# Optimization experiments

Measured on AMD Instinct MI355X. Metric: run time of the kernel, lower is better.

Reference implementation:

```python
import jax, jax.numpy as jnp
import numpy as np

B, S, HID = 1, 2048, 2048
NH, NKV, HD = 16, 4, 128
G = NH // NKV  # queries per kv head (repeat_interleave factor)
QPA = 128      # query_pre_attn_scalar
EPS = 1e-6
SCALE = QPA ** -0.5
NEG = -1e9


def rms_norm(x, w, eps=EPS):
    return x * jax.lax.rsqrt(jnp.mean(x * x, axis=-1, keepdims=True) + eps) * w


def rope(x, cos, sin):
    # x: [B,S,H,D]; cos/sin: [S,D/2].
    # torch apply_rotary_emb: complex (x[:d/2] + i*x[d/2:]) * (cos + i*sin),
    # real parts -> first half, imag parts -> second half.
    d2 = x.shape[-1] // 2
    x1, x2 = x[..., :d2], x[..., d2:]
    c = cos[None, :, None, :]
    s = sin[None, :, None, :]
    return jnp.concatenate([x1 * c - x2 * s, x1 * s + x2 * c], axis=-1)


def setup_inputs() -> dict:
    key = jax.random.key(0)
    ks = jax.random.split(key, 4)
    hidden_states = jax.random.normal(ks[0], (B, S, HID), jnp.float32)
    inv_freq = 1.0 / (10000.0 ** (jnp.arange(0, HD, 2, dtype=jnp.float32) / HD))
    ang = jnp.arange(S, dtype=jnp.float32)[:, None] * inv_freq[None, :]  # [S, D/2]
    cos, sin = jnp.cos(ang), jnp.sin(ang)
    kv_write_indices = jnp.arange(S, dtype=jnp.int32)
    k_cache = jnp.zeros((B, S, NKV, HD), jnp.float32)
    v_cache = jnp.zeros((B, S, NKV, HD), jnp.float32)
    causal = jnp.tril(jnp.ones((S, S), dtype=bool))
    mask = jnp.where(causal, 0.0, NEG).astype(jnp.float32)[None, None]  # [1,1,S,S]
    qkv_out = (NH + 2 * NKV) * HD
    wqkv = jax.random.normal(ks[1], (qkv_out, HID), jnp.float32) * 0.02
    bqkv = jnp.zeros((qkv_out,), jnp.float32)
    wo = jax.random.normal(ks[2], (HID, NH * HD), jnp.float32) * 0.02
    bo = jnp.zeros((HID,), jnp.float32)
    q_norm_w = jnp.ones((HD,), jnp.float32)
    k_norm_w = jnp.ones((HD,), jnp.float32)
    return {"hidden_states": hidden_states, "cos": cos, "sin": sin,
            "k_cache": k_cache, "v_cache": v_cache, "mask": mask,
            "wqkv": wqkv, "bqkv": bqkv, "wo": wo, "bo": bo,
            "q_norm_w": q_norm_w, "k_norm_w": k_norm_w,
            "kv_write_indices": kv_write_indices}


def reference(hidden_states, cos, sin, k_cache, v_cache, mask,
              wqkv, bqkv, wo, bo, q_norm_w, k_norm_w, kv_write_indices):
    qkv = hidden_states @ wqkv.T + bqkv  # [B,S,(NH+2*NKV)*HD]
    q_sz, kv_sz = NH * HD, NKV * HD
    xq = qkv[..., :q_sz].reshape(B, S, NH, HD)
    xk = qkv[..., q_sz:q_sz + kv_sz].reshape(B, S, NKV, HD)
    xv = qkv[..., q_sz + kv_sz:].reshape(B, S, NKV, HD)
    xq = rope(rms_norm(xq, q_norm_w), cos, sin)
    xk = rope(rms_norm(xk, k_norm_w), cos, sin)
    k = k_cache.at[:, kv_write_indices].set(xk)  # index_copy_ on dim 1
    v = v_cache.at[:, kv_write_indices].set(xv)
    # GQA: head h attends with kv head h // G (repeat_interleave order)
    q = (xq * SCALE).reshape(B, S, NKV, G, HD)
    scores = jnp.einsum('bskgd,btkd->bkgst', q, k) + mask[:, :, None]  # [B,NKV,G,S,T]
    p = jax.nn.softmax(scores.astype(jnp.float32), axis=-1).astype(q.dtype)
    out = jnp.einsum('bkgst,btkd->bskgd', p, v).reshape(B, S, NH * HD)
    return out @ wo.T + bo
```

## Files before the change

kernel.cpp:

```cpp
#include <hip/hip_runtime.h>
#include <stdint.h>

#define S_LEN 2048
#define HIDN  2048
#define NH    16
#define NKV   4
#define HD    128
#define QKV_N 3072
#define Q_SZ  2048
#define SCALE_Q 0.088388347648318447f

typedef __attribute__((ext_vector_type(8))) short  short8;
typedef __attribute__((ext_vector_type(4))) float  f32x4;

__device__ __forceinline__ uint16_t f2bf(float f) {
  uint32_t u = __float_as_uint(f);
  u += 0x7fffu + ((u >> 16) & 1u);
  return (uint16_t)(u >> 16);
}

__device__ __forceinline__ void gload16(const void* g, void* lds_wave_base) {
  __builtin_amdgcn_global_load_lds(
      (const __attribute__((address_space(1))) uint32_t*)(uintptr_t)g,
      (__attribute__((address_space(3))) uint32_t*)(uint32_t)(uintptr_t)lds_wave_base,
      16, 0, 0);
}

__global__ __launch_bounds__(256) void cvt_kernel(const float* __restrict__ in,
                                                  uint16_t* __restrict__ out, int n) {
  int i = (blockIdx.x * 256 + threadIdx.x) * 4;
  if (i < n) {
    float4 v = *(const float4*)(in + i);
    ushort4 o;
    o.x = f2bf(v.x); o.y = f2bf(v.y); o.z = f2bf(v.z); o.w = f2bf(v.w);
    *(ushort4*)(out + i) = o;
  }
}

#define BM 128
#define BN 128
#define BK 64
__global__ __launch_bounds__(256) void gemm_nt(const uint16_t* __restrict__ A,
                                               const uint16_t* __restrict__ B,
                                               const float* __restrict__ bias,
                                               float* __restrict__ C,
                                               int M, int N, int K) {
  __shared__ uint16_t As[BM * BK];
  __shared__ uint16_t Bs[BN * BK];
  const int tid = threadIdx.x;
  const int m0 = blockIdx.y * BM;
  const int n0 = blockIdx.x * BN;
  const int lane = tid & 63;
  const int w = tid >> 6;
  const int wm = (w >> 1) * 64, wn = (w & 1) * 64;
  const int lr = lane & 15, lg = lane >> 4;
  const int wb = w << 10;
  const int lb = wb + lane * 16;

  f32x4 acc[4][4];
#pragma unroll
  for (int i = 0; i < 4; ++i)
#pragma unroll
    for (int j = 0; j < 4; ++j) acc[i][j] = (f32x4){0.f, 0.f, 0.f, 0.f};

  for (int k0 = 0; k0 < K; k0 += BK) {
#pragma unroll
    for (int i = 0; i < 4; ++i) {
      int b = i * 4096 + lb;
      int row = b >> 7;
      int colb = b & 127;
      gload16((const char*)A + ((size_t)(m0 + row) * K + k0) * 2 + colb,
              (char*)As + i * 4096 + wb);
      gload16((const char*)B + ((size_t)(n0 + row) * K + k0) * 2 + colb,
              (char*)Bs + i * 4096 + wb);
    }
    __syncthreads();
#pragma unroll
    for (int ks = 0; ks < 2; ++ks) {
      short8 av[4], bv[4];
#pragma unroll
      for (int i = 0; i < 4; ++i)
        av[i] = *(const short8*)(As + (wm + i * 16 + lr) * BK + ks * 32 + lg * 8);
#pragma unroll
      for (int j = 0; j < 4; ++j)
        bv[j] = *(const short8*)(Bs + (wn + j * 16 + lr) * BK + ks * 32 + lg * 8);
#pragma unroll
      for (int i = 0; i < 4; ++i)
#pragma unroll
        for (int j = 0; j < 4; ++j)
          acc[i][j] = __builtin_amdgcn_mfma_f32_16x16x32_bf16(av[i], bv[j], acc[i][j], 0, 0, 0);
    }
    __syncthreads();
  }
#pragma unroll
  for (int i = 0; i < 4; ++i) {
#pragma unroll
    for (int j = 0; j < 4; ++j) {
      int col = n0 + wn + j * 16 + lr;
      float bb = bias ? bias[col] : 0.f;
#pragma unroll
      for (int r = 0; r < 4; ++r) {
        int rowg = m0 + wm + i * 16 + lg * 4 + r;
        C[(size_t)rowg * N + col] = acc[i][j][r] + bb;
      }
    }
  }
}

__global__ __launch_bounds__(256) void qk_post(const float* __restrict__ qkv,
                                               const float* __restrict__ cosb,
                                               const float* __restrict__ sinb,
                                               const float* __restrict__ qw,
                                               const float* __restrict__ kw,
                                               const int* __restrict__ widx,
                                               uint16_t* __restrict__ Qo,
                                               uint16_t* __restrict__ Ko) {
  int row = blockIdx.x * 4 + (threadIdx.x >> 6);
  int lane = threadIdx.x & 63;
  int t = row / 20, head = row % 20;
  bool isq = head < NH;
  int off = isq ? head * HD : Q_SZ + (head - NH) * HD;
  const float* x = qkv + (size_t)t * QKV_N + off;
  float x1 = x[lane], x2 = x[lane + 64];
  float ss = x1 * x1 + x2 * x2;
#pragma unroll
  for (int m = 1; m < 64; m <<= 1) ss += __shfl_xor(ss, m, 64);
  float rs = rsqrtf(ss * (1.0f / 128.0f) + 1e-6f);
  const float* wn_ = isq ? qw : kw;
  float n1 = x1 * rs * wn_[lane], n2 = x2 * rs * wn_[lane + 64];
  float c = cosb[t * 64 + lane], s = sinb[t * 64 + lane];
  float o1 = n1 * c - n2 * s;
  float o2 = n1 * s + n2 * c;
  if (isq) {
    o1 *= SCALE_Q; o2 *= SCALE_Q;
    uint16_t* dst = Qo + ((size_t)t * NH + head) * HD;
    dst[lane] = f2bf(o1); dst[lane + 64] = f2bf(o2);
  } else {
    int td = widx[t];
    uint16_t* dst = Ko + ((size_t)td * NKV + (head - NH)) * HD;
    dst[lane] = f2bf(o1); dst[lane + 64] = f2bf(o2);
  }
}

__global__ __launch_bounds__(256) void vtrans(const float* __restrict__ qkv,
                                              const int* __restrict__ widx,
                                              uint16_t* __restrict__ Vt) {
  int b = blockIdx.x;
  int dt = b & 1;
  int tt = (b >> 1) & 31;
  int kh = b >> 6;
  __shared__ float tile[64][68];
  int tid = threadIdx.x;
  int r = tid >> 2, c0 = tid & 3;
  const float* src = qkv + (size_t)(tt * 64 + r) * QKV_N + Q_SZ + NKV * HD + kh * HD + dt * 64;
#pragma unroll
  for (int i = 0; i < 4; ++i) {
    float4 v = *(const float4*)(src + (c0 + i * 4) * 4);
    *(float4*)&tile[r][(c0 + i * 4) * 4] = v;
  }
  __syncthreads();
  int rd = tid >> 2;
#pragma unroll
  for (int j = 0; j < 16; ++j) {
    int tloc = c0 * 16 + j;
    int tg = widx[tt * 64 + tloc];
    Vt[(size_t)(kh * HD + dt * 64 + rd) * S_LEN + tg] = f2bf(tile[tloc][rd]);
  }
}

__global__ __launch_bounds__(256) void attn_kernel(const uint16_t* __restrict__ Q,
                                                   const uint16_t* __restrict__ Kc,
                                                   const uint16_t* __restrict__ Vt,
                                                   uint16_t* __restrict__ O) {
  __shared__ uint16_t Ks[64 * 128];
  __shared__ uint16_t Vs[128 * 64];
  __shared__ uint16_t Ps[4][16 * 136];
  __shared__ float Bc[4][16];

  const int h = blockIdx.y, kh = h >> 2;
  const int q0 = blockIdx.x * 64;
  const int tid = threadIdx.x, w = tid >> 6, lane = tid & 63;
  const int lr = lane & 15, lg = lane >> 4;
  const int qw0 = q0 + w * 16;
  const int wb = w << 10, lb = wb + lane * 16;

  short8 qf[4];
  const uint16_t* qb = Q + ((size_t)(qw0 + lr) * NH + h) * HD;
#pragma unroll
  for (int ks = 0; ks < 4; ++ks) qf[ks] = *(const short8*)(qb + ks * 32 + lg * 8);

  f32x4 o[8];
#pragma unroll
  for (int d = 0; d < 8; ++d) o[d] = (f32x4){0.f, 0.f, 0.f, 0.f};
  float mrun = -1e30f, lrun = 0.f;
  const int qg = qw0 + lr;

  const int ntiles = q0 / 64 + 1;
  for (int tt = 0; tt < ntiles; ++tt) {
    const int t0 = tt * 64;
#pragma unroll
    for (int i = 0; i < 4; ++i) {
      int b = i * 4096 + lb;
      int rowK = b >> 8, colK = b & 255;
      gload16((const char*)Kc + (((size_t)(t0 + rowK) * NKV + kh) * HD) * 2 + (colK ^ ((rowK & 7) << 4)),
              (char*)Ks + i * 4096 + wb);
      int rowV = b >> 7, colV = b & 127;
      gload16((const char*)Vt + ((size_t)(kh * HD + rowV) * S_LEN + t0) * 2 + (colV ^ ((rowV & 7) << 4)),
              (char*)Vs + i * 4096 + wb);
    }
    __syncthreads();

    f32x4 st[4];
#pragma unroll
    for (int ts = 0; ts < 4; ++ts) {
      st[ts] = (f32x4){0.f, 0.f, 0.f, 0.f};
#pragma unroll
      for (int ks = 0; ks < 4; ++ks) {
        int row = ts * 16 + lr;
        int cb = (ks * 64 + lg * 16) ^ ((row & 7) << 4);
        short8 kf = *(const short8*)((const char*)Ks + row * 256 + cb);
        st[ts] = __builtin_amdgcn_mfma_f32_16x16x32_bf16(kf, qf[ks], st[ts], 0, 0, 0);
      }
    }

    float pv[4][4];
    float pm = -1e30f;
#pragma unroll
    for (int ts = 0; ts < 4; ++ts)
#pragma unroll
      for (int r = 0; r < 4; ++r) {
        int tglob = t0 + ts * 16 + lg * 4 + r;
        float sv = (tglob > qg) ? -1e9f : st[ts][r];
        pv[ts][r] = sv;
        pm = fmaxf(pm, sv);
      }
    pm = fmaxf(pm, __shfl_xor(pm, 16, 64));
    pm = fmaxf(pm, __shfl_xor(pm, 32, 64));
    float mnew = fmaxf(mrun, pm);
    float scl = __expf(mrun - mnew);
    float psum = 0.f;
#pragma unroll
    for (int ts = 0; ts < 4; ++ts)
#pragma unroll
      for (int r = 0; r < 4; ++r) {
        pv[ts][r] = __expf(pv[ts][r] - mnew);
        psum += pv[ts][r];
      }
    psum += __shfl_xor(psum, 16, 64);
    psum += __shfl_xor(psum, 32, 64);
    lrun = lrun * scl + psum;
    mrun = mnew;
    if (lg == 0) Bc[w][lr] = scl;

    {
      uint32_t* pw = (uint32_t*)&Ps[w][0];
#pragma unroll
      for (int ts = 0; ts < 4; ++ts)
#pragma unroll
        for (int rr = 0; rr < 2; ++rr) {
          uint32_t pp = (uint32_t)f2bf(pv[ts][2 * rr]) | ((uint32_t)f2bf(pv[ts][2 * rr + 1]) << 16);
          pw[lr * 68 + ts * 8 + lg * 2 + rr] = pp;
        }
    }
    __syncthreads();

#pragma unroll
    for (int r = 0; r < 4; ++r) {
      float s4 = Bc[w][lg * 4 + r];
#pragma unroll
      for (int d = 0; d < 8; ++d) o[d][r] *= s4;
    }
#pragma unroll
    for (int ks = 0; ks < 2; ++ks) {
      short8 pf = *(const short8*)((const char*)&Ps[w][0] + lr * 272 + ks * 64 + lg * 16);
#pragma unroll
      for (int d = 0; d < 8; ++d) {
        int row = d * 16 + lr;
        int cb = (ks * 64 + lg * 16) ^ ((row & 7) << 4);
        short8 vf = *(const short8*)((const char*)Vs + row * 128 + cb);
        o[d] = __builtin_amdgcn_mfma_f32_16x16x32_bf16(pf, vf, o[d], 0, 0, 0);
      }
    }
    __syncthreads();
  }

  if (lg == 0) Bc[w][lr] = lrun;
  __syncthreads();
#pragma unroll
  for (int r = 0; r < 4; ++r) {
    float inv = 1.0f / Bc[w][lg * 4 + r];
    int qg2 = qw0 + lg * 4 + r;
    uint16_t* dst = O + ((size_t)qg2 * NH + h) * HD;
#pragma unroll
    for (int d = 0; d < 8; ++d) dst[d * 16 + lr] = f2bf(o[d][r] * inv);
  }
}

extern "C" void kernel_launch(void* const* d_in, const int* in_sizes, int n_in,
                              void* d_out, int out_size, void* d_ws, size_t ws_size,
                              hipStream_t stream) {
  const float* hidden = (const float*)d_in[0];
  const float* cosb   = (const float*)d_in[1];
  const float* sinb   = (const float*)d_in[2];
  const float* wqkv = (const float*)d_in[6];
  const float* bqkv = (const float*)d_in[7];
  const float* wo   = (const float*)d_in[8];
  const float* bo   = (const float*)d_in[9];
  const float* qnw  = (const float*)d_in[10];
  const float* knw  = (const float*)d_in[11];
  const int*   widx = (const int*)d_in[12];
  float* out = (float*)d_out;

  char* ws = (char*)d_ws;
  uint16_t* hb    = (uint16_t*)(ws);
  uint16_t* wqb   = (uint16_t*)(ws + (8u  << 20));
  uint16_t* wob   = (uint16_t*)(ws + (20u << 20));
  float*    qkv   = (float*)   (ws + (28u << 20));
  uint16_t* Qb    = (uint16_t*)(ws + (52u << 20));
  uint16_t* Kb    = (uint16_t*)(ws + (60u << 20));
  uint16_t* Vtb   = (uint16_t*)(ws + (62u << 20));
  uint16_t* attnb = (uint16_t*)(ws);

  cvt_kernel<<<4096, 256, 0, stream>>>(hidden, hb, S_LEN * HIDN);
  cvt_kernel<<<6144, 256, 0, stream>>>(wqkv, wqb, QKV_N * HIDN);
  cvt_kernel<<<4096, 256, 0, stream>>>(wo, wob, HIDN * HIDN);

  gemm_nt<<<dim3(QKV_N / BN, S_LEN / BM), 256, 0, stream>>>(hb, wqb, bqkv, qkv,
                                                            S_LEN, QKV_N, HIDN);
  qk_post<<<S_LEN * 20 / 4, 256, 0, stream>>>(qkv, cosb, sinb, qnw, knw, widx, Qb, Kb);
  vtrans<<<NKV * (S_LEN / 64) * (HD / 64), 256, 0, stream>>>(qkv, widx, Vtb);
  attn_kernel<<<dim3(S_LEN / 64, NH), 256, 0, stream>>>(Qb, Kb, Vtb, attnb);
  gemm_nt<<<dim3(HIDN / BN, S_LEN / BM), 256, 0, stream>>>(attnb, wob, bo, out,
                                                           S_LEN, HIDN, HIDN);
}
```

Before: 314.2 us.

## Double-buffer GEMM and attention tiles, fuse conversions, reorder Q/K layout

Merges the three fp32-to-bf16 conversion launches into one kernel. Both GEMMs move to 512 threads with double-buffered LDS, so the next K tile loads while the current one computes. Attention gains double-buffered K/V tiles, applies the causal mask only on the diagonal tile, launches heaviest query tiles first, and moves Q/K to a head-major layout. It also swizzles the P buffer, passes row scale and sum by shuffles instead of LDS with a barrier, and raises wave priority around the MFMA sections. Costs are more LDS per block, which may lower occupancy, and a larger set of simultaneous changes.

```diff
diff --git a/kernel.cpp b/kernel.cpp
--- a/kernel.cpp
+++ b/kernel.cpp
@@ -26,76 +26,87 @@
       16, 0, 0);
 }
 
-__global__ __launch_bounds__(256) void cvt_kernel(const float* __restrict__ in,
-                                                  uint16_t* __restrict__ out, int n) {
+__global__ __launch_bounds__(256) void cvt3_kernel(const float* __restrict__ a, uint16_t* __restrict__ oa, int na,
+                                                   const float* __restrict__ b, uint16_t* __restrict__ ob, int nb,
+                                                   const float* __restrict__ c, uint16_t* __restrict__ oc, int nc) {
   int i = (blockIdx.x * 256 + threadIdx.x) * 4;
-  if (i < n) {
-    float4 v = *(const float4*)(in + i);
-    ushort4 o;
-    o.x = f2bf(v.x); o.y = f2bf(v.y); o.z = f2bf(v.z); o.w = f2bf(v.w);
-    *(ushort4*)(out + i) = o;
-  }
+  const float* src; uint16_t* dst; int j;
+  if (i < na)           { src = a; dst = oa; j = i; }
+  else if (i < na + nb) { src = b; dst = ob; j = i - na; }
+  else if (i < na + nb + nc) { src = c; dst = oc; j = i - na - nb; }
+  else return;
+  float4 v = *(const float4*)(src + j);
+  ushort4 o;
+  o.x = f2bf(v.x); o.y = f2bf(v.y); o.z = f2bf(v.z); o.w = f2bf(v.w);
+  *(ushort4*)(dst + j) = o;
 }
 
 #define BM 128
 #define BN 128
 #define BK 64
-__global__ __launch_bounds__(256) void gemm_nt(const uint16_t* __restrict__ A,
+__global__ __launch_bounds__(512) void gemm_nt(const uint16_t* __restrict__ A,
                                                const uint16_t* __restrict__ B,
                                                const float* __restrict__ bias,
                                                float* __restrict__ C,
                                                int M, int N, int K) {
-  __shared__ uint16_t As[BM * BK];
-  __shared__ uint16_t Bs[BN * BK];
+  __shared__ uint16_t As[2][BM * BK];
+  __shared__ uint16_t Bs[2][BN * BK];
   const int tid = threadIdx.x;
   const int m0 = blockIdx.y * BM;
   const int n0 = blockIdx.x * BN;
   const int lane = tid & 63;
   const int w = tid >> 6;
-  const int wm = (w >> 1) * 64, wn = (w & 1) * 64;
+  const int wm = (w >> 2) * 64, wn = (w & 3) * 32;
   const int lr = lane & 15, lg = lane >> 4;
   const int wb = w << 10;
   const int lb = wb + lane * 16;
 
-  f32x4 acc[4][4];
+  f32x4 acc[4][2];
 #pragma unroll
   for (int i = 0; i < 4; ++i)
 #pragma unroll
-    for (int j = 0; j < 4; ++j) acc[i][j] = (f32x4){0.f, 0.f, 0.f, 0.f};
-
-  for (int k0 = 0; k0 < K; k0 += BK) {
-#pragma unroll
-    for (int i = 0; i < 4; ++i) {
-      int b = i * 4096 + lb;
-      int row = b >> 7;
-      int colb = b & 127;
+    for (int j = 0; j < 2; ++j) acc[i][j] = (f32x4){0.f, 0.f, 0.f, 0.f};
+
+  auto stage = [&](int buf, int k0) {
+#pragma unroll
+    for (int i = 0; i < 2; ++i) {
+      int bofs = i * 8192 + lb;
+      int row = bofs >> 7;
+      int colb = bofs & 127;
       gload16((const char*)A + ((size_t)(m0 + row) * K + k0) * 2 + colb,
-              (char*)As + i * 4096 + wb);
+              (char*)As[buf] + i * 8192 + wb);
       gload16((const char*)B + ((size_t)(n0 + row) * K + k0) * 2 + colb,
-              (char*)Bs + i * 4096 + wb);
+              (char*)Bs[buf] + i * 8192 + wb);
+    }
+  };
+
+  stage(0, 0);
+  __syncthreads();
+  const int nk = K / BK;
+  for (int kk = 0; kk < nk; ++kk) {
+    const int cur = kk & 1;
+    if (kk + 1 < nk) stage(cur ^ 1, (kk + 1) * BK);
+#pragma unroll
+    for (int ks = 0; ks < 2; ++ks) {
+      short8 av[4], bv[2];
+#pragma unroll
+      for (int i = 0; i < 4; ++i)
+        av[i] = *(const short8*)(As[cur] + (wm + i * 16 + lr) * BK + ks * 32 + lg * 8);
+#pragma unroll
+      for (int j = 0; j < 2; ++j)
+        bv[j] = *(const short8*)(Bs[cur] + (wn + j * 16 + lr) * BK + ks * 32 + lg * 8);
+#pragma unroll
+      for (int i = 0; i < 4; ++i)
+#pragma unroll
+        for (int j = 0; j < 2; ++j)
+          acc[i][j] = __builtin_amdgcn_mfma_f32_16x16x32_bf16(av[i], bv[j], acc[i][j], 0, 0, 0);
     }
     __syncthreads();
-#pragma unroll
-    for (int ks = 0; ks < 2; ++ks) {
-      short8 av[4], bv[4];
-#pragma unroll
-      for (int i = 0; i < 4; ++i)
-        av[i] = *(const short8*)(As + (wm + i * 16 + lr) * BK + ks * 32 + lg * 8);
-#pragma unroll
-      for (int j = 0; j < 4; ++j)
-        bv[j] = *(const short8*)(Bs + (wn + j * 16 + lr) * BK + ks * 32 + lg * 8);
-#pragma unroll
-      for (int i = 0; i < 4; ++i)
-#pragma unroll
-        for (int j = 0; j < 4; ++j)
-          acc[i][j] = __builtin_amdgcn_mfma_f32_16x16x32_bf16(av[i], bv[j], acc[i][j], 0, 0, 0);
-    }
-    __syncthreads();
   }
 #pragma unroll
   for (int i = 0; i < 4; ++i) {
 #pragma unroll
-    for (int j = 0; j < 4; ++j) {
+    for (int j = 0; j < 2; ++j) {
       int col = n0 + wn + j * 16 + lr;
       float bb = bias ? bias[col] : 0.f;
 #pragma unroll
@@ -133,11 +144,11 @@
   float o2 = n1 * s + n2 * c;
   if (isq) {
     o1 *= SCALE_Q; o2 *= SCALE_Q;
-    uint16_t* dst = Qo + ((size_t)t * NH + head) * HD;
+    uint16_t* dst = Qo + ((size_t)head * S_LEN + t) * HD;
     dst[lane] = f2bf(o1); dst[lane + 64] = f2bf(o2);
   } else {
     int td = widx[t];
-    uint16_t* dst = Ko + ((size_t)td * NKV + (head - NH)) * HD;
+    uint16_t* dst = Ko + ((size_t)(head - NH) * S_LEN + td) * HD;
     dst[lane] = f2bf(o1); dst[lane + 64] = f2bf(o2);
   }
 }
@@ -172,20 +183,20 @@
                                                    const uint16_t* __restrict__ Kc,
                                                    const uint16_t* __restrict__ Vt,
                                                    uint16_t* __restrict__ O) {
-  __shared__ uint16_t Ks[64 * 128];
-  __shared__ uint16_t Vs[128 * 64];
-  __shared__ uint16_t Ps[4][16 * 136];
-  __shared__ float Bc[4][16];
+  __shared__ uint16_t Ks[2][64 * 128];
+  __shared__ uint16_t Vs[2][128 * 64];
+  __shared__ uint16_t Ps[4][16 * 64];
 
   const int h = blockIdx.y, kh = h >> 2;
-  const int q0 = blockIdx.x * 64;
+  const int qt = (S_LEN / 64 - 1) - blockIdx.x;
+  const int q0 = qt * 64;
   const int tid = threadIdx.x, w = tid >> 6, lane = tid & 63;
   const int lr = lane & 15, lg = lane >> 4;
   const int qw0 = q0 + w * 16;
   const int wb = w << 10, lb = wb + lane * 16;
 
   short8 qf[4];
-  const uint16_t* qb = Q + ((size_t)(qw0 + lr) * NH + h) * HD;
+  const uint16_t* qb = Q + ((size_t)h * S_LEN + qw0 + lr) * HD;
 #pragma unroll
   for (int ks = 0; ks < 4; ++ks) qf[ks] = *(const short8*)(qb + ks * 32 + lg * 8);
 
@@ -195,22 +206,30 @@
   float mrun = -1e30f, lrun = 0.f;
   const int qg = qw0 + lr;
 
-  const int ntiles = q0 / 64 + 1;
-  for (int tt = 0; tt < ntiles; ++tt) {
-    const int t0 = tt * 64;
+  auto stage = [&](int buf, int t0) {
 #pragma unroll
     for (int i = 0; i < 4; ++i) {
       int b = i * 4096 + lb;
       int rowK = b >> 8, colK = b & 255;
-      gload16((const char*)Kc + (((size_t)(t0 + rowK) * NKV + kh) * HD) * 2 + (colK ^ ((rowK & 7) << 4)),
-              (char*)Ks + i * 4096 + wb);
+      gload16((const char*)Kc + ((size_t)kh * S_LEN + t0 + rowK) * (HD * 2) + (colK ^ ((rowK & 7) << 4)),
+              (char*)Ks[buf] + i * 4096 + wb);
       int rowV = b >> 7, colV = b & 127;
       gload16((const char*)Vt + ((size_t)(kh * HD + rowV) * S_LEN + t0) * 2 + (colV ^ ((rowV & 7) << 4)),
-              (char*)Vs + i * 4096 + wb);
-    }
-    __syncthreads();
+              (char*)Vs[buf] + i * 4096 + wb);
+    }
+  };
+
+  const int ntiles = qt + 1;
+  stage(0, 0);
+  __syncthreads();
+
+  for (int tt = 0; tt < ntiles; ++tt) {
+    const int cur = tt & 1;
+    const int t0 = tt * 64;
+    if (tt + 1 < ntiles) stage(cur ^ 1, t0 + 64);
 
     f32x4 st[4];
+    __builtin_amdgcn_s_setprio(1);
 #pragma unroll
     for (int ts = 0; ts < 4; ++ts) {
       st[ts] = (f32x4){0.f, 0.f, 0.f, 0.f};
@@ -218,22 +237,33 @@
       for (int ks = 0; ks < 4; ++ks) {
         int row = ts * 16 + lr;
         int cb = (ks * 64 + lg * 16) ^ ((row & 7) << 4);
-        short8 kf = *(const short8*)((const char*)Ks + row * 256 + cb);
+        short8 kf = *(const short8*)((const char*)Ks[cur] + row * 256 + cb);
         st[ts] = __builtin_amdgcn_mfma_f32_16x16x32_bf16(kf, qf[ks], st[ts], 0, 0, 0);
       }
     }
-
-    float pv[4][4];
+    __builtin_amdgcn_s_setprio(0);
+
+    float pvv[4][4];
     float pm = -1e30f;
-#pragma unroll
-    for (int ts = 0; ts < 4; ++ts)
-#pragma unroll
-      for (int r = 0; r < 4; ++r) {
-        int tglob = t0 + ts * 16 + lg * 4 + r;
-        float sv = (tglob > qg) ? -1e9f : st[ts][r];
-        pv[ts][r] = sv;
-        pm = fmaxf(pm, sv);
-      }
+    if (tt == ntiles - 1) {
+#pragma unroll
+      for (int ts = 0; ts < 4; ++ts)
+#pragma unroll
+        for (int r = 0; r < 4; ++r) {
+          int tglob = t0 + ts * 16 + lg * 4 + r;
+          float sv = (tglob > qg) ? -1e9f : st[ts][r];
+          pvv[ts][r] = sv;
+          pm = fmaxf(pm, sv);
+        }
+    } else {
+#pragma unroll
+      for (int ts = 0; ts < 4; ++ts)
+#pragma unroll
+        for (int r = 0; r < 4; ++r) {
+          pvv[ts][r] = st[ts][r];
+          pm = fmaxf(pm, st[ts][r]);
+        }
+    }
     pm = fmaxf(pm, __shfl_xor(pm, 16, 64));
     pm = fmaxf(pm, __shfl_xor(pm, 32, 64));
     float mnew = fmaxf(mrun, pm);
@@ -243,14 +273,13 @@
     for (int ts = 0; ts < 4; ++ts)
 #pragma unroll
       for (int r = 0; r < 4; ++r) {
-        pv[ts][r] = __expf(pv[ts][r] - mnew);
-        psum += pv[ts][r];
+        pvv[ts][r] = __expf(pvv[ts][r] - mnew);
+        psum += pvv[ts][r];
       }
     psum += __shfl_xor(psum, 16, 64);
     psum += __shfl_xor(psum, 32, 64);
     lrun = lrun * scl + psum;
     mrun = mnew;
-    if (lg == 0) Bc[w][lr] = scl;
 
     {
       uint32_t* pw = (uint32_t*)&Ps[w][0];
@@ -258,37 +287,39 @@
       for (int ts = 0; ts < 4; ++ts)
 #pragma unroll
         for (int rr = 0; rr < 2; ++rr) {
-          uint32_t pp = (uint32_t)f2bf(pv[ts][2 * rr]) | ((uint32_t)f2bf(pv[ts][2 * rr + 1]) << 16);
-          pw[lr * 68 + ts * 8 + lg * 2 + rr] = pp;
+          uint32_t pp = (uint32_t)f2bf(pvv[ts][2 * rr]) | ((uint32_t)f2bf(pvv[ts][2 * rr + 1]) << 16);
+          pw[lr * 32 + ((ts * 8 + lg * 2 + rr) ^ ((lr & 7) << 2))] = pp;
         }
     }
-    __syncthreads();
 
 #pragma unroll
     for (int r = 0; r < 4; ++r) {
-      float s4 = Bc[w][lg * 4 + r];
+      float s4 = __shfl(scl, (lane & 48) | (lg * 4 + r), 64);
 #pragma unroll
       for (int d = 0; d < 8; ++d) o[d][r] *= s4;
     }
+
+    __builtin_amdgcn_s_setprio(1);
 #pragma unroll
     for (int ks = 0; ks < 2; ++ks) {
-      short8 pf = *(const short8*)((const char*)&Ps[w][0] + lr * 272 + ks * 64 + lg * 16);
+      short8 pf = *(const short8*)((const char*)&Ps[w][0] + lr * 128 + ((ks * 64 + lg * 16) ^ ((lr & 7) << 4)));
 #pragma unroll
       for (int d = 0; d < 8; ++d) {
         int row = d * 16 + lr;
         int cb = (ks * 64 + lg * 16) ^ ((row & 7) << 4);
-        short8 vf = *(const short8*)((const char*)Vs + row * 128 + cb);
+        short8 vf = *(const short8*)((const char*)Vs[cur] + row * 128 + cb);
         o[d] = __builtin_amdgcn_mfma_f32_16x16x32_bf16(pf, vf, o[d], 0, 0, 0);
       }
     }
+    __builtin_amdgcn_s_setprio(0);
+
     __syncthreads();
   }
 
-  if (lg == 0) Bc[w][lr] = lrun;
-  __syncthreads();
 #pragma unroll
   for (int r = 0; r < 4; ++r) {
-    float inv = 1.0f / Bc[w][lg * 4 + r];
+    float ls = __shfl(lrun, (lane & 48) | (lg * 4 + r), 64);
+    float inv = 1.0f / ls;
     int qg2 = qw0 + lg * 4 + r;
     uint16_t* dst = O + ((size_t)qg2 * NH + h) * HD;
 #pragma unroll
@@ -321,15 +352,14 @@
   uint16_t* Vtb   = (uint16_t*)(ws + (62u << 20));
   uint16_t* attnb = (uint16_t*)(ws);
 
-  cvt_kernel<<<4096, 256, 0, stream>>>(hidden, hb, S_LEN * HIDN);
-  cvt_kernel<<<6144, 256, 0, stream>>>(wqkv, wqb, QKV_N * HIDN);
-  cvt_kernel<<<4096, 256, 0, stream>>>(wo, wob, HIDN * HIDN);
-
-  gemm_nt<<<dim3(QKV_N / BN, S_LEN / BM), 256, 0, stream>>>(hb, wqb, bqkv, qkv,
+  const int na = S_LEN * HIDN, nb = QKV_N * HIDN, nc = HIDN * HIDN;
+  cvt3_kernel<<<(na + nb + nc) / 4 / 256, 256, 0, stream>>>(hidden, hb, na, wqkv, wqb, nb, wo, wob, nc);
+
+  gemm_nt<<<dim3(QKV_N / BN, S_LEN / BM), 512, 0, stream>>>(hb, wqb, bqkv, qkv,
                                                             S_LEN, QKV_N, HIDN);
   qk_post<<<S_LEN * 20 / 4, 256, 0, stream>>>(qkv, cosb, sinb, qnw, knw, widx, Qb, Kb);
   vtrans<<<NKV * (S_LEN / 64) * (HD / 64), 256, 0, stream>>>(qkv, widx, Vtb);
   attn_kernel<<<dim3(S_LEN / 64, NH), 256, 0, stream>>>(Qb, Kb, Vtb, attnb);
-  gemm_nt<<<dim3(HIDN / BN, S_LEN / BM), 256, 0, stream>>>(attnb, wob, bo, out,
+  gemm_nt<<<dim3(HIDN / BN, S_LEN / BM), 512, 0, stream>>>(attnb, wob, bo, out,
                                                            S_LEN, HIDN, HIDN);
 }
```

Result: faster. 297.8 us (-5.2%).
